# Optimization experiments

Hardware: AMD Instinct MI355X
Metric: run time of the kernel (lower is better)

Reference implementation:

```python
import jax, jax.numpy as jnp
import numpy as np

F = 26          # number of sparse features / tables
D = 128         # shared embedding_dim
N = 100000      # num_embeddings per table
B = 4096        # batch size (KJT stride)
L = 20          # average pooling length
T = B * L       # total indices per feature (fixed for static shapes)


def setup_inputs() -> dict:
    key = jax.random.key(0)
    k_tab, k_val, k_off = jax.random.split(key, 3)
    # Learned embedding tables: [F, N, D]
    tables = jax.random.normal(k_tab, (F, N, D), dtype=jnp.float32) * 0.01
    # Jagged index values per feature: [F, T]
    values = jax.random.randint(k_val, (F, T), 0, N, dtype=jnp.int64)
    # Offsets per feature: [F, B+1], sorted, fixed endpoints 0 and T (ragged bag lengths)
    inner = jnp.sort(jax.random.randint(k_off, (F, B - 1), 0, T, dtype=jnp.int64), axis=1)
    zeros = jnp.zeros((F, 1), dtype=jnp.int64)
    tops = jnp.full((F, 1), T, dtype=jnp.int64)
    offsets = jnp.concatenate([zeros, inner, tops], axis=1)
    return {"tables": tables, "values": values, "offsets": offsets}


def reference(tables, values, offsets):
    # Per-feature pooled (SUM) EmbeddingBag over jagged offsets, then concat -> [B, F, D]
    pos = jnp.arange(T)

    def per_feature(tab, vals, offs):
        emb = tab[vals]  # gather: [T, D]
        # bag id for each index position: offs[j] <= i < offs[j+1] -> segment j
        seg = jnp.searchsorted(offs, pos, side="right") - 1  # [T]
        return jax.ops.segment_sum(emb, seg, num_segments=B)  # [B, D]

    pooled = jax.vmap(per_feature)(tables, values, offsets)  # [F, B, D]
    # torch.cat(per-feature [B,D], dim=1).reshape(B, F, D) == stack on axis=1
    return jnp.transpose(pooled, (1, 0, 2))  # [B, F, D]
```

## Files before the change

kernel.cpp:

```cpp
#include <hip/hip_runtime.h>

#define NUM_F   26
#define DIM     128
#define NROWS   100000
#define BATCH   4096
#define TLEN    81920

__global__ __launch_bounds__(256) void ebag_kernel(
    const float* __restrict__ tables,
    const int*   __restrict__ values,
    const int*   __restrict__ offsets,
    float*       __restrict__ out)
{
    const int wid  = blockIdx.x * 4 + (threadIdx.x >> 6);
    const int lane = threadIdx.x & 63;
    if (wid >= NUM_F * BATCH) return;

    const int f = wid >> 12;
    const int b = wid & (BATCH - 1);

    const int off_base = f * (BATCH + 1) + b;
    const int start = offsets[off_base];
    const int end   = offsets[off_base + 1];

    const float* __restrict__ tab  = tables + (size_t)f * NROWS * DIM;
    const int*   __restrict__ vals = values + (size_t)f * TLEN;

    const int      hi   = lane >> 5;
    const unsigned colB = (unsigned)(lane & 31) * 16u;

    float a0 = 0.0f, a1 = 0.0f, a2 = 0.0f, a3 = 0.0f;

#define PAIR_LOAD(vv, jj)                                                   \
    {                                                                       \
        const int iA = __builtin_amdgcn_readlane(myidx, (jj));              \
        const int iB = __builtin_amdgcn_readlane(myidx, (jj) + 1);          \
        const int row = hi ? iB : iA;                                       \
        const unsigned off = ((unsigned)row << 9) + colB;                   \
        vv = *(const float4*)((const char*)tab + off);                      \
    }

    for (int i0 = start; i0 < end; i0 += 64) {
        const int cnt = min(64, end - i0);
        int myidx = 0;
        if (i0 + lane < end) myidx = vals[i0 + lane];

        int j = 0;
        for (; j + 16 <= cnt; j += 16) {
            float4 v0, v1, v2, v3, v4, v5, v6, v7;
            PAIR_LOAD(v0, j + 0);
            PAIR_LOAD(v1, j + 2);
            PAIR_LOAD(v2, j + 4);
            PAIR_LOAD(v3, j + 6);
            PAIR_LOAD(v4, j + 8);
            PAIR_LOAD(v5, j + 10);
            PAIR_LOAD(v6, j + 12);
            PAIR_LOAD(v7, j + 14);
            a0 += (v0.x + v1.x) + (v2.x + v3.x) + (v4.x + v5.x) + (v6.x + v7.x);
            a1 += (v0.y + v1.y) + (v2.y + v3.y) + (v4.y + v5.y) + (v6.y + v7.y);
            a2 += (v0.z + v1.z) + (v2.z + v3.z) + (v4.z + v5.z) + (v6.z + v7.z);
            a3 += (v0.w + v1.w) + (v2.w + v3.w) + (v4.w + v5.w) + (v6.w + v7.w);
        }
        for (; j + 2 <= cnt; j += 2) {
            float4 v0;
            PAIR_LOAD(v0, j);
            a0 += v0.x; a1 += v0.y; a2 += v0.z; a3 += v0.w;
        }
        if (j < cnt) {
            const int iA = __builtin_amdgcn_readlane(myidx, j);
            if (lane < 32) {
                const unsigned off = ((unsigned)iA << 9) + colB;
                const float4 v = *(const float4*)((const char*)tab + off);
                a0 += v.x; a1 += v.y; a2 += v.z; a3 += v.w;
            }
        }
    }
#undef PAIR_LOAD

    a0 += __shfl_xor(a0, 32);
    a1 += __shfl_xor(a1, 32);
    a2 += __shfl_xor(a2, 32);
    a3 += __shfl_xor(a3, 32);

    if (lane < 32) {
        float4 r; r.x = a0; r.y = a1; r.z = a2; r.w = a3;
        ((float4*)(out + ((size_t)b * NUM_F + f) * DIM))[lane] = r;
    }
}

extern "C" void kernel_launch(void* const* d_in, const int* in_sizes, int n_in,
                              void* d_out, int out_size, void* d_ws, size_t ws_size,
                              hipStream_t stream) {
    const float* tables  = (const float*)d_in[0];
    const int*   values  = (const int*)d_in[1];
    const int*   offsets = (const int*)d_in[2];
    float*       out     = (float*)d_out;

    const int total_waves = NUM_F * BATCH;
    const int blocks = total_waves / 4;
    ebag_kernel<<<dim3(blocks), dim3(256), 0, stream>>>(tables, values, offsets, out);
}
```

Measured before the change: 1.588 ms.

## Parallelize over fixed 64-index chunks with binary-search segments and boundary atomics

```diff
diff --git a/kernel.cpp b/kernel.cpp
--- a/kernel.cpp
+++ b/kernel.cpp
@@ -5,8 +5,17 @@
 #define NROWS   100000
 #define BATCH   4096
 #define TLEN    81920
+#define CHUNKS_PER_F (TLEN / 64)
 
-__global__ __launch_bounds__(256) void ebag_kernel(
+__global__ __launch_bounds__(256) void zero_out_kernel(float4* __restrict__ out4, int n4)
+{
+    int i = blockIdx.x * blockDim.x + threadIdx.x;
+    const int stride = gridDim.x * blockDim.x;
+    const float4 z = {0.f, 0.f, 0.f, 0.f};
+    for (; i < n4; i += stride) out4[i] = z;
+}
+
+__global__ __launch_bounds__(256) void ebag_seg_kernel(
     const float* __restrict__ tables,
     const int*   __restrict__ values,
     const int*   __restrict__ offsets,
@@ -14,77 +23,68 @@
 {
     const int wid  = blockIdx.x * 4 + (threadIdx.x >> 6);
     const int lane = threadIdx.x & 63;
-    if (wid >= NUM_F * BATCH) return;
 
-    const int f = wid >> 12;
-    const int b = wid & (BATCH - 1);
+    const int f = wid / CHUNKS_PER_F;
+    const int c = wid - f * CHUNKS_PER_F;
+    const int cstart = c * 64;
+    const int pos = cstart + lane;
 
-    const int off_base = f * (BATCH + 1) + b;
-    const int start = offsets[off_base];
-    const int end   = offsets[off_base + 1];
+    const int*   __restrict__ vals = values  + f * TLEN;
+    const int*   __restrict__ offs = offsets + f * (BATCH + 1);
+    const float* __restrict__ tab  = tables  + (size_t)f * NROWS * DIM;
 
-    const float* __restrict__ tab  = tables + (size_t)f * NROWS * DIM;
-    const int*   __restrict__ vals = values + (size_t)f * TLEN;
+    const int myidx = vals[pos];
 
-    const int      hi   = lane >> 5;
-    const unsigned colB = (unsigned)(lane & 31) * 16u;
+    int lo = 0, hi = BATCH;
+    #pragma unroll
+    for (int it = 0; it < 12; ++it) {
+        const int m = (lo + hi) >> 1;
+        if (offs[m] <= pos) lo = m; else hi = m;
+    }
+    const int myseg = lo;
 
-    float a0 = 0.0f, a1 = 0.0f, a2 = 0.0f, a3 = 0.0f;
+    const int prev = __shfl_up(myseg, 1);
+    const unsigned long long bmask = __ballot(myseg != prev) | 1ull;
 
-#define PAIR_LOAD(vv, jj)                                                   \
-    {                                                                       \
-        const int iA = __builtin_amdgcn_readlane(myidx, (jj));              \
-        const int iB = __builtin_amdgcn_readlane(myidx, (jj) + 1);          \
-        const int row = hi ? iB : iA;                                       \
-        const unsigned off = ((unsigned)row << 9) + colB;                   \
-        vv = *(const float4*)((const char*)tab + off);                      \
-    }
+    const unsigned colB = (unsigned)lane * 8u;
+    float ax = 0.f, ay = 0.f;
 
-    for (int i0 = start; i0 < end; i0 += 64) {
-        const int cnt = min(64, end - i0);
-        int myidx = 0;
-        if (i0 + lane < end) myidx = vals[i0 + lane];
+    int j = 0;
+    while (j < 64) {
+        const unsigned long long rest = (j < 63) ? (bmask >> (j + 1)) : 0ull;
+        const int next = rest ? (j + 1 + __builtin_ctzll(rest)) : 64;
+        const int s = __builtin_amdgcn_readlane(myseg, j);
 
-        int j = 0;
-        for (; j + 16 <= cnt; j += 16) {
-            float4 v0, v1, v2, v3, v4, v5, v6, v7;
-            PAIR_LOAD(v0, j + 0);
-            PAIR_LOAD(v1, j + 2);
-            PAIR_LOAD(v2, j + 4);
-            PAIR_LOAD(v3, j + 6);
-            PAIR_LOAD(v4, j + 8);
-            PAIR_LOAD(v5, j + 10);
-            PAIR_LOAD(v6, j + 12);
-            PAIR_LOAD(v7, j + 14);
-            a0 += (v0.x + v1.x) + (v2.x + v3.x) + (v4.x + v5.x) + (v6.x + v7.x);
-            a1 += (v0.y + v1.y) + (v2.y + v3.y) + (v4.y + v5.y) + (v6.y + v7.y);
-            a2 += (v0.z + v1.z) + (v2.z + v3.z) + (v4.z + v5.z) + (v6.z + v7.z);
-            a3 += (v0.w + v1.w) + (v2.w + v3.w) + (v4.w + v5.w) + (v6.w + v7.w);
+        int k = j;
+        for (; k + 4 <= next; k += 4) {
+            const int i0 = __builtin_amdgcn_readlane(myidx, k + 0);
+            const int i1 = __builtin_amdgcn_readlane(myidx, k + 1);
+            const int i2 = __builtin_amdgcn_readlane(myidx, k + 2);
+            const int i3 = __builtin_amdgcn_readlane(myidx, k + 3);
+            const float2 v0 = *(const float2*)((const char*)tab + (((unsigned)i0 << 9) + colB));
+            const float2 v1 = *(const float2*)((const char*)tab + (((unsigned)i1 << 9) + colB));
+            const float2 v2 = *(const float2*)((const char*)tab + (((unsigned)i2 << 9) + colB));
+            const float2 v3 = *(const float2*)((const char*)tab + (((unsigned)i3 << 9) + colB));
+            ax += (v0.x + v1.x) + (v2.x + v3.x);
+            ay += (v0.y + v1.y) + (v2.y + v3.y);
         }
-        for (; j + 2 <= cnt; j += 2) {
-            float4 v0;
-            PAIR_LOAD(v0, j);
-            a0 += v0.x; a1 += v0.y; a2 += v0.z; a3 += v0.w;
+        for (; k < next; ++k) {
+            const int idx = __builtin_amdgcn_readlane(myidx, k);
+            const float2 v = *(const float2*)((const char*)tab + (((unsigned)idx << 9) + colB));
+            ax += v.x;
+            ay += v.y;
         }
-        if (j < cnt) {
-            const int iA = __builtin_amdgcn_readlane(myidx, j);
-            if (lane < 32) {
-                const unsigned off = ((unsigned)iA << 9) + colB;
-                const float4 v = *(const float4*)((const char*)tab + off);
-                a0 += v.x; a1 += v.y; a2 += v.z; a3 += v.w;
-            }
+
+        float* ob = out + ((size_t)s * NUM_F + f) * DIM + (lane * 2);
+        if (j == 0 || next == 64) {
+            atomicAdd(ob + 0, ax);
+            atomicAdd(ob + 1, ay);
+        } else {
+            float2 r; r.x = ax; r.y = ay;
+            *(float2*)ob = r;
         }
-    }
-#undef PAIR_LOAD
-
-    a0 += __shfl_xor(a0, 32);
-    a1 += __shfl_xor(a1, 32);
-    a2 += __shfl_xor(a2, 32);
-    a3 += __shfl_xor(a3, 32);
-
-    if (lane < 32) {
-        float4 r; r.x = a0; r.y = a1; r.z = a2; r.w = a3;
-        ((float4*)(out + ((size_t)b * NUM_F + f) * DIM))[lane] = r;
+        ax = 0.f; ay = 0.f;
+        j = next;
     }
 }
 
@@ -96,7 +96,10 @@
     const int*   offsets = (const int*)d_in[2];
     float*       out     = (float*)d_out;
 
-    const int total_waves = NUM_F * BATCH;
+    const int n4 = BATCH * NUM_F * DIM / 4;
+    zero_out_kernel<<<dim3(1024), dim3(256), 0, stream>>>((float4*)out, n4);
+
+    const int total_waves = NUM_F * CHUNKS_PER_F;
     const int blocks = total_waves / 4;
-    ebag_kernel<<<dim3(blocks), dim3(256), 0, stream>>>(tables, values, offsets, out);
+    ebag_seg_kernel<<<dim3(blocks), dim3(256), 0, stream>>>(tables, values, offsets, out);
 }
```

New measurement: 1.605 ms. Within noise of the previous version (+1.1%).
